# Kernel optimization log

Hardware: AMD Instinct MI355X
Metric: run time of the kernel (lower is better)

## Reference

```python
import jax, jax.numpy as jnp
import numpy as np

N = 4096            # number of proposals
C = 6               # classes incl. background
SCORE_TH = 0.05
NMS_TH = 0.3
DET_LIM = 100
IM_MAX = 1023.0     # clip to [0, im_size-1]
BBOX_W = jnp.array([10.0, 10.0, 10.0, 5.0, 5.0, 5.0], dtype=jnp.float32)


def setup_inputs() -> dict:
    key = jax.random.key(0)
    k1, k2, k3, k4 = jax.random.split(key, 4)
    # realistic 3D proposals inside the 1024^3 volume: lo in [0,900), size in [1,101)
    lo = jax.random.uniform(k1, (N, 3), dtype=jnp.float32) * 900.0
    sz = jax.random.uniform(k2, (N, 3), dtype=jnp.float32) * 100.0 + 1.0
    bbox_proposals = jnp.concatenate([jnp.zeros((N, 1), jnp.float32), lo, lo + sz], axis=1)  # [N,7]
    bbox_pred = jax.random.normal(k3, (N, C * 6), dtype=jnp.float32) * 0.1                   # [N,36]
    cls_score = jax.random.normal(k4, (N, C), dtype=jnp.float32)                              # [N,6]
    return {"bbox_proposals": bbox_proposals, "bbox_pred": bbox_pred, "cls_score": cls_score}


def _bbox_transform_clip(boxes, deltas):
    # boxes: [N,6] (x1,y1,z1,x2,y2,z2); deltas: [N, C*6] -> pred_boxes [N,C,6]
    d = deltas.reshape(N, C, 6) / BBOX_W
    sizes = boxes[:, 3:6] - boxes[:, 0:3] + 1.0          # [N,3]
    ctrs = boxes[:, 0:3] + 0.5 * sizes                   # [N,3]
    pred_ctr = d[:, :, :3] * sizes[:, None, :] + ctrs[:, None, :]
    pred_sz = jnp.exp(d[:, :, 3:]) * sizes[:, None, :]
    lo = jnp.clip(pred_ctr - 0.5 * pred_sz, 0.0, IM_MAX)
    hi = jnp.clip(pred_ctr + 0.5 * pred_sz - 1.0, 0.0, IM_MAX)
    return jnp.concatenate([lo, hi], axis=-1)            # [N,C,6]


def _nms_one_class(bj, sj):
    # bj: [N,6], sj: [N] -> scores with suppressed/below-threshold entries zeroed
    valid = sj > SCORE_TH
    order = jnp.argsort(-sj)
    b = bj[order]
    v = valid[order]
    l, h = b[:, :3], b[:, 3:]
    vol = jnp.prod(h - l + 1.0, axis=1)                                  # [N]
    inter = jnp.prod(
        jnp.clip(jnp.minimum(h[:, None, :], h[None, :, :])
                 - jnp.maximum(l[:, None, :], l[None, :, :]) + 1.0, 0.0, None),
        axis=-1)                                                          # [N,N]
    iou = inter / (vol[:, None] + vol[None, :] - inter)
    idx = jnp.arange(N)

    def body(i, keep):
        supp = keep[i] & (iou[i] > NMS_TH) & (idx > i)
        return keep & ~supp

    keep = jax.lax.fori_loop(0, N, body, v)
    keep_orig = jnp.zeros(N, bool).at[order].set(keep)
    return jnp.where(keep_orig, sj, 0.0)


def reference(bbox_proposals, bbox_pred, cls_score):
    scores = jax.nn.softmax(cls_score, axis=1)            # [N,C]
    boxes = bbox_proposals[:, 1:]                          # [N,6]
    pred_boxes = _bbox_transform_clip(boxes, bbox_pred)    # [N,C,6]
    cls_boxes = jnp.transpose(pred_boxes[:, 1:, :], (1, 0, 2))  # [5,N,6] (skip background)
    cls_scores = scores[:, 1:].T                                 # [5,N]
    kept = jax.vmap(_nms_one_class)(cls_boxes, cls_scores)       # [5,N]
    # top-100 detections-per-image limit (fixed-shape: zero out below image_thresh)
    thresh = jax.lax.top_k(kept.reshape(-1), DET_LIM)[0][-1]
    final = jnp.where(kept >= thresh, kept, 0.0)
    # pack boxes + final score: [5, N, 7]
    return jnp.concatenate([cls_boxes, final[:, :, None]], axis=-1)
```

## Files before the change

### kernel.cpp

```cpp
#include <hip/hip_runtime.h>
#include <stdint.h>

#define NN 4096
#define NCLS 5
#define NWORD 64
#define SCORE_TH 0.05f
#define NMS_TH 0.3f

__device__ __forceinline__ uint32_t fmap(float f) {
    uint32_t u = __float_as_uint(f);
    return (u & 0x80000000u) ? ~u : (u | 0x80000000u);
}
__device__ __forceinline__ float funmap(uint32_t m) {
    uint32_t u = (m & 0x80000000u) ? (m & 0x7fffffffu) : ~m;
    return __uint_as_float(u);
}

__global__ void k_prep(const float* __restrict__ prop, const float* __restrict__ pred,
                       const float* __restrict__ cls, float* __restrict__ out,
                       uint64_t* __restrict__ skey) {
    int i = blockIdx.x * 256 + threadIdx.x;
    if (i >= NN) return;
    const float* pr = prop + i * 7;
    float l0 = pr[1], l1 = pr[2], l2 = pr[3];
    float h0 = pr[4], h1 = pr[5], h2 = pr[6];
    float s0 = h0 - l0 + 1.f, s1 = h1 - l1 + 1.f, s2 = h2 - l2 + 1.f;
    float c0 = l0 + 0.5f * s0, c1 = l1 + 0.5f * s1, c2 = l2 + 0.5f * s2;

    float sc[6];
    float mx = -3.4e38f;
#pragma unroll
    for (int c = 0; c < 6; ++c) { sc[c] = cls[i * 6 + c]; mx = fmaxf(mx, sc[c]); }
    float sum = 0.f;
#pragma unroll
    for (int c = 0; c < 6; ++c) { sc[c] = expf(sc[c] - mx); sum += sc[c]; }
    float inv = 1.f / sum;

#pragma unroll
    for (int c = 1; c < 6; ++c) {
        const float* d = pred + i * 36 + c * 6;
        float dc0 = d[0] / 10.f, dc1 = d[1] / 10.f, dc2 = d[2] / 10.f;
        float ds0 = d[3] / 5.f, ds1 = d[4] / 5.f, ds2 = d[5] / 5.f;
        float pc0 = dc0 * s0 + c0, pc1 = dc1 * s1 + c1, pc2 = dc2 * s2 + c2;
        float ps0 = expf(ds0) * s0, ps1 = expf(ds1) * s1, ps2 = expf(ds2) * s2;
        float o0 = fminf(fmaxf(pc0 - 0.5f * ps0, 0.f), 1023.f);
        float o1 = fminf(fmaxf(pc1 - 0.5f * ps1, 0.f), 1023.f);
        float o2 = fminf(fmaxf(pc2 - 0.5f * ps2, 0.f), 1023.f);
        float o3 = fminf(fmaxf(pc0 + 0.5f * ps0 - 1.f, 0.f), 1023.f);
        float o4 = fminf(fmaxf(pc1 + 0.5f * ps1 - 1.f, 0.f), 1023.f);
        float o5 = fminf(fmaxf(pc2 + 0.5f * ps2 - 1.f, 0.f), 1023.f);
        float* ob = out + ((size_t)(c - 1) * NN + i) * 7;
        ob[0] = o0; ob[1] = o1; ob[2] = o2; ob[3] = o3; ob[4] = o4; ob[5] = o5;
        float score = sc[c] * inv;
        skey[(c - 1) * NN + i] = ((uint64_t)fmap(score) << 12) | (uint32_t)(4095 - i);
    }
}

__global__ void __launch_bounds__(256) k_sort(const uint64_t* __restrict__ skey,
                                              const float* __restrict__ out,
                                              float* __restrict__ sscores,
                                              unsigned short* __restrict__ order,
                                              float* __restrict__ sboxes) {
    int c = blockIdx.y;
    int i = blockIdx.x * 256 + threadIdx.x;
    const uint64_t* K = skey + c * NN;
    uint64_t ki = K[i];
    int rank = 0;
#pragma unroll 2
    for (int j = 0; j < NN; j += 8) {
        uint64_t k0 = K[j], k1 = K[j + 1], k2 = K[j + 2], k3 = K[j + 3];
        uint64_t k4 = K[j + 4], k5 = K[j + 5], k6 = K[j + 6], k7 = K[j + 7];
        int a = (k0 > ki) + (k1 > ki) + (k2 > ki) + (k3 > ki);
        int b = (k4 > ki) + (k5 > ki) + (k6 > ki) + (k7 > ki);
        rank += a + b;
    }
    int io = c * NN + rank;
    order[io] = (unsigned short)i;
    sscores[io] = funmap((uint32_t)(ki >> 12));
    const float* b = out + ((size_t)c * NN + i) * 7;
    float* sb = sboxes + (size_t)io * 6;
#pragma unroll
    for (int k = 0; k < 6; ++k) sb[k] = b[k];
}

__global__ void __launch_bounds__(256) k_mask(const float* __restrict__ sboxes,
                                              uint64_t* __restrict__ mask,
                                              uint64_t* __restrict__ diag) {
    int tid = threadIdx.x;
    int wid = tid >> 6, lane = tid & 63;
    int rb = blockIdx.y, c = blockIdx.z;
    int cb = rb + blockIdx.x * 4 + wid;
    bool active = (cb < 64);

    __shared__ float cB[4][64][6];
    __shared__ float cV[4][64];

    int r = rb * 64 + lane;
    float rl0 = 0, rl1 = 0, rl2 = 0, rh0 = 0, rh1 = 0, rh2 = 0, vi = 0;
    if (active) {
        const float* rp = sboxes + ((size_t)c * NN + r) * 6;
        rl0 = rp[0]; rl1 = rp[1]; rl2 = rp[2];
        rh0 = rp[3]; rh1 = rp[4]; rh2 = rp[5];
        vi = (rh0 - rl0 + 1.f) * (rh1 - rl1 + 1.f) * (rh2 - rl2 + 1.f);
        const float* cp = sboxes + ((size_t)c * NN + cb * 64 + lane) * 6;
#pragma unroll
        for (int k = 0; k < 6; ++k) cB[wid][lane][k] = cp[k];
        cV[wid][lane] = (cB[wid][lane][3] - cB[wid][lane][0] + 1.f) *
                        (cB[wid][lane][4] - cB[wid][lane][1] + 1.f) *
                        (cB[wid][lane][5] - cB[wid][lane][2] + 1.f);
    }
    __syncthreads();
    if (!active) return;

    uint64_t bits = 0;
    for (int j2 = 0; j2 < 64; ++j2) {
        int j = cb * 64 + j2;
        if (j > r) {
            float w0 = fmaxf(fminf(rh0, cB[wid][j2][3]) - fmaxf(rl0, cB[wid][j2][0]) + 1.f, 0.f);
            float w1 = fmaxf(fminf(rh1, cB[wid][j2][4]) - fmaxf(rl1, cB[wid][j2][1]) + 1.f, 0.f);
            float w2 = fmaxf(fminf(rh2, cB[wid][j2][5]) - fmaxf(rl2, cB[wid][j2][2]) + 1.f, 0.f);
            float inter = w0 * w1 * w2;
            float iou = inter / (vi + cV[wid][j2] - inter);
            if (iou > NMS_TH) bits |= 1ull << j2;
        }
    }
    mask[((size_t)c * NN + r) * NWORD + cb] = bits;
    if (cb == rb) diag[(size_t)c * NN + r] = bits;
}

__global__ void __launch_bounds__(64, 1) k_nms(const float* __restrict__ sscores,
                                               const unsigned short* __restrict__ order,
                                               const uint64_t* __restrict__ mask,
                                               const uint64_t* __restrict__ diag,
                                               float* __restrict__ kept) {
    __shared__ __align__(16) uint64_t ldiag[NN];
    __shared__ uint64_t sh[64];

    int c = blockIdx.x;
    int lane = threadIdx.x;
    const uint64_t* M = mask + (size_t)c * NN * NWORD;
    const uint64_t* D = diag + (size_t)c * NN;
    const float* ss = sscores + c * NN;

    {
        const uint4* g = (const uint4*)D;
        uint4* l = (uint4*)ldiag;
#pragma unroll 1
        for (int i = 0; i < 32; i += 8) {
            uint4 t0 = g[(i + 0) * 64 + lane], t1 = g[(i + 1) * 64 + lane];
            uint4 t2 = g[(i + 2) * 64 + lane], t3 = g[(i + 3) * 64 + lane];
            uint4 t4 = g[(i + 4) * 64 + lane], t5 = g[(i + 5) * 64 + lane];
            uint4 t6 = g[(i + 6) * 64 + lane], t7 = g[(i + 7) * 64 + lane];
            l[(i + 0) * 64 + lane] = t0; l[(i + 1) * 64 + lane] = t1;
            l[(i + 2) * 64 + lane] = t2; l[(i + 3) * 64 + lane] = t3;
            l[(i + 4) * 64 + lane] = t4; l[(i + 5) * 64 + lane] = t5;
            l[(i + 6) * 64 + lane] = t6; l[(i + 7) * 64 + lane] = t7;
        }
    }

    uint64_t remv = 0;
    {
        const float4* sl = (const float4*)(ss + lane * 64);
#pragma unroll
        for (int q = 0; q < 16; ++q) {
            float4 v = sl[q];
            if (!(v.x > SCORE_TH)) remv |= 1ull << (q * 4);
            if (!(v.y > SCORE_TH)) remv |= 1ull << (q * 4 + 1);
            if (!(v.z > SCORE_TH)) remv |= 1ull << (q * 4 + 2);
            if (!(v.w > SCORE_TH)) remv |= 1ull << (q * 4 + 3);
        }
    }
    __builtin_amdgcn_s_barrier();

#define ISSUE16(buf, base)                                          \
    _Pragma("unroll") for (int i_ = 0; i_ < 16; ++i_) {             \
        buf[i_] = R[(((base) + i_) << 6) | lane];                   \
    }

#define CHAIN16(base)                                               \
    {                                                               \
        uint32_t lo_[16], hi_[16];                                  \
        _Pragma("unroll") for (int b_ = 0; b_ < 16; ++b_) {         \
            lo_[b_] = __builtin_amdgcn_readlane(dgl, (base) + b_);  \
            hi_[b_] = __builtin_amdgcn_readlane(dgh, (base) + b_);  \
        }                                                           \
        _Pragma("unroll") for (int b_ = 0; b_ < 16; ++b_) {         \
            int bb_ = (base) + b_;                                  \
            if (!((rw >> bb_) & 1)) {                               \
                rw |= ((uint64_t)hi_[b_] << 32) | lo_[b_];          \
                kmask |= 1ull << bb_;                               \
            }                                                       \
        }                                                           \
    }

#define CONSUME16(buf, base, acc)                                   \
    _Pragma("unroll") for (int i_ = 0; i_ < 16; ++i_) {             \
        uint64_t kb_ = 0ull - ((kmask >> ((base) + i_)) & 1ull);    \
        acc |= buf[i_] & kb_;                                       \
    }

#pragma unroll 1
    for (int w = 0; w < 64; ++w) {
        const uint64_t* R = M + ((size_t)w << 12);
        uint64_t gA[16], gB[16];

        ISSUE16(gA, 0)
        ISSUE16(gB, 16)
        __builtin_amdgcn_sched_barrier(0);

        uint32_t rlo = __builtin_amdgcn_readlane((uint32_t)remv, w);
        uint32_t rhi = __builtin_amdgcn_readlane((uint32_t)(remv >> 32), w);
        uint64_t rw = ((uint64_t)rhi << 32) | rlo;
        uint64_t mydg = ldiag[(w << 6) | lane];
        uint32_t dgl = (uint32_t)mydg, dgh = (uint32_t)(mydg >> 32);
        uint64_t kmask = 0;
        uint64_t a0 = 0, a1 = 0, a2 = 0, a3 = 0;

        CHAIN16(0)
        CONSUME16(gA, 0, a0)
        ISSUE16(gA, 32)
        CHAIN16(16)
        CONSUME16(gB, 16, a1)
        ISSUE16(gB, 48)
        CHAIN16(32)
        CONSUME16(gA, 32, a2)
        CHAIN16(48)
        CONSUME16(gB, 48, a3)

        if (lane >= w) remv |= (a0 | a1) | (a2 | a3);
    }

#undef ISSUE16
#undef CHAIN16
#undef CONSUME16

    sh[lane] = remv;
    __syncthreads();
    const unsigned short* ord = order + c * NN;
    for (int t = 0; t < 64; ++t) {
        int p = t * 64 + lane;
        bool kp = !((sh[t] >> lane) & 1);
        float s = ss[p];
        int oi = ord[p];
        kept[c * NN + oi] = kp ? s : 0.f;
    }
}

__global__ void __launch_bounds__(1024) k_topk_final(const float* __restrict__ kept,
                                                     float* __restrict__ out) {
    int tid = threadIdx.x;
    uint32_t v[20];
#pragma unroll
    for (int k = 0; k < 20; ++k) v[k] = fmap(kept[k * 1024 + tid]);
    __shared__ int red[16];
    __shared__ int tot;
    uint32_t pre = 0;
    for (int bit = 31; bit >= 0; --bit) {
        uint32_t cand = pre | (1u << bit);
        int cnt = 0;
#pragma unroll
        for (int k = 0; k < 20; ++k) cnt += (v[k] >= cand);
#pragma unroll
        for (int off = 32; off; off >>= 1) cnt += __shfl_down(cnt, off, 64);
        if ((tid & 63) == 0) red[tid >> 6] = cnt;
        __syncthreads();
        if (tid == 0) {
            int s = 0;
            for (int q = 0; q < 16; ++q) s += red[q];
            tot = s;
        }
        __syncthreads();
        if (tot >= 100) pre = cand;
    }
#pragma unroll
    for (int k = 0; k < 20; ++k) {
        int idx = k * 1024 + tid;
        int c = idx >> 12;
        int i = idx & (NN - 1);
        out[((size_t)c * NN + i) * 7 + 6] = (v[k] >= pre) ? funmap(v[k]) : 0.f;
    }
}

extern "C" void kernel_launch(void* const* d_in, const int* in_sizes, int n_in,
                              void* d_out, int out_size, void* d_ws, size_t ws_size,
                              hipStream_t stream) {
    const float* prop = (const float*)d_in[0];
    const float* pred = (const float*)d_in[1];
    const float* cls = (const float*)d_in[2];
    float* out = (float*)d_out;

    char* base = (char*)d_ws;
    uint64_t* skey = (uint64_t*)base;
    uint64_t* diag = (uint64_t*)(base + (160ull << 10));
    float* sscores = (float*)(base + (320ull << 10));
    float* kept = (float*)(base + (400ull << 10));
    unsigned short* order = (unsigned short*)(base + (480ull << 10));
    float* sboxes = (float*)(base + (528ull << 10));
    uint64_t* mask = (uint64_t*)(base + (1ull << 20));

    k_prep<<<dim3(16), dim3(256), 0, stream>>>(prop, pred, cls, out, skey);
    k_sort<<<dim3(16, NCLS), dim3(256), 0, stream>>>(skey, out, sscores, order, sboxes);
    k_mask<<<dim3(16, 64, NCLS), dim3(256), 0, stream>>>(sboxes, mask, diag);
    k_nms<<<dim3(NCLS), dim3(64), 0, stream>>>(sscores, order, mask, diag, kept);
    k_topk_final<<<dim3(1), dim3(1024), 0, stream>>>(kept, out);
}
```

Before: 411.6 us.

## Split NMS bitmask scan across four wavefronts with LDS-shared keep mask

The serial NMS scan kernel now runs four wavefronts per class instead of one. Wave 0 resolves the 64-bit keep chain for each block, and all waves OR their own 16-row slice of the suppression mask. Partial suppression words pass through LDS slots, and each step prefetches the next block's mask rows. The goal is to spread mask loads and OR work over more waves and hide load latency. In exchange it adds two workgroup barriers per iteration on the serial critical path.

```diff
diff --git a/kernel.cpp b/kernel.cpp
--- a/kernel.cpp
+++ b/kernel.cpp
@@ -128,16 +128,27 @@
     if (cb == rb) diag[(size_t)c * NN + r] = bits;
 }
 
-__global__ void __launch_bounds__(64, 1) k_nms(const float* __restrict__ sscores,
-                                               const unsigned short* __restrict__ order,
-                                               const uint64_t* __restrict__ mask,
-                                               const uint64_t* __restrict__ diag,
-                                               float* __restrict__ kept) {
+#define NMS_BARRIER()                                        \
+    do {                                                     \
+        asm volatile("s_waitcnt lgkmcnt(0)" ::: "memory");   \
+        __builtin_amdgcn_s_barrier();                        \
+        asm volatile("" ::: "memory");                       \
+    } while (0)
+
+__global__ void __launch_bounds__(256, 1) k_nms(const float* __restrict__ sscores,
+                                                const unsigned short* __restrict__ order,
+                                                const uint64_t* __restrict__ mask,
+                                                const uint64_t* __restrict__ diag,
+                                                float* __restrict__ kept) {
     __shared__ __align__(16) uint64_t ldiag[NN];
+    __shared__ uint64_t slot[4];
+    __shared__ uint64_t pacc[4][64];
     __shared__ uint64_t sh[64];
-
+    __shared__ uint32_t km_sh[2];
+
+    int tid = threadIdx.x;
+    int wid = tid >> 6, lane = tid & 63;
     int c = blockIdx.x;
-    int lane = threadIdx.x;
     const uint64_t* M = mask + (size_t)c * NN * NWORD;
     const uint64_t* D = diag + (size_t)c * NN;
     const float* ss = sscores + c * NN;
@@ -145,37 +156,35 @@
     {
         const uint4* g = (const uint4*)D;
         uint4* l = (uint4*)ldiag;
-#pragma unroll 1
-        for (int i = 0; i < 32; i += 8) {
-            uint4 t0 = g[(i + 0) * 64 + lane], t1 = g[(i + 1) * 64 + lane];
-            uint4 t2 = g[(i + 2) * 64 + lane], t3 = g[(i + 3) * 64 + lane];
-            uint4 t4 = g[(i + 4) * 64 + lane], t5 = g[(i + 5) * 64 + lane];
-            uint4 t6 = g[(i + 6) * 64 + lane], t7 = g[(i + 7) * 64 + lane];
-            l[(i + 0) * 64 + lane] = t0; l[(i + 1) * 64 + lane] = t1;
-            l[(i + 2) * 64 + lane] = t2; l[(i + 3) * 64 + lane] = t3;
-            l[(i + 4) * 64 + lane] = t4; l[(i + 5) * 64 + lane] = t5;
-            l[(i + 6) * 64 + lane] = t6; l[(i + 7) * 64 + lane] = t7;
-        }
-    }
-
-    uint64_t remv = 0;
-    {
+        uint4 t0 = g[(wid * 8 + 0) * 64 + lane], t1 = g[(wid * 8 + 1) * 64 + lane];
+        uint4 t2 = g[(wid * 8 + 2) * 64 + lane], t3 = g[(wid * 8 + 3) * 64 + lane];
+        uint4 t4 = g[(wid * 8 + 4) * 64 + lane], t5 = g[(wid * 8 + 5) * 64 + lane];
+        uint4 t6 = g[(wid * 8 + 6) * 64 + lane], t7 = g[(wid * 8 + 7) * 64 + lane];
+        l[(wid * 8 + 0) * 64 + lane] = t0; l[(wid * 8 + 1) * 64 + lane] = t1;
+        l[(wid * 8 + 2) * 64 + lane] = t2; l[(wid * 8 + 3) * 64 + lane] = t3;
+        l[(wid * 8 + 4) * 64 + lane] = t4; l[(wid * 8 + 5) * 64 + lane] = t5;
+        l[(wid * 8 + 6) * 64 + lane] = t6; l[(wid * 8 + 7) * 64 + lane] = t7;
+    }
+
+    uint64_t initW = 0;
+    if (wid == 0) {
         const float4* sl = (const float4*)(ss + lane * 64);
 #pragma unroll
         for (int q = 0; q < 16; ++q) {
             float4 v = sl[q];
-            if (!(v.x > SCORE_TH)) remv |= 1ull << (q * 4);
-            if (!(v.y > SCORE_TH)) remv |= 1ull << (q * 4 + 1);
-            if (!(v.z > SCORE_TH)) remv |= 1ull << (q * 4 + 2);
-            if (!(v.w > SCORE_TH)) remv |= 1ull << (q * 4 + 3);
-        }
-    }
-    __builtin_amdgcn_s_barrier();
-
-#define ISSUE16(buf, base)                                          \
-    _Pragma("unroll") for (int i_ = 0; i_ < 16; ++i_) {             \
-        buf[i_] = R[(((base) + i_) << 6) | lane];                   \
-    }
+            if (!(v.x > SCORE_TH)) initW |= 1ull << (q * 4);
+            if (!(v.y > SCORE_TH)) initW |= 1ull << (q * 4 + 1);
+            if (!(v.z > SCORE_TH)) initW |= 1ull << (q * 4 + 2);
+            if (!(v.w > SCORE_TH)) initW |= 1ull << (q * 4 + 3);
+        }
+    }
+    if (tid < 4) slot[tid] = 0;
+
+    uint64_t g0[16];
+#pragma unroll
+    for (int i = 0; i < 16; ++i) g0[i] = M[((wid * 16 + i) << 6) | lane];
+
+    NMS_BARRIER();
 
 #define CHAIN16(base)                                               \
     {                                                               \
@@ -193,51 +202,55 @@
         }                                                           \
     }
 
-#define CONSUME16(buf, base, acc)                                   \
-    _Pragma("unroll") for (int i_ = 0; i_ < 16; ++i_) {             \
-        uint64_t kb_ = 0ull - ((kmask >> ((base) + i_)) & 1ull);    \
-        acc |= buf[i_] & kb_;                                       \
-    }
-
+    uint64_t racc = 0;
 #pragma unroll 1
     for (int w = 0; w < 64; ++w) {
-        const uint64_t* R = M + ((size_t)w << 12);
-        uint64_t gA[16], gB[16];
-
-        ISSUE16(gA, 0)
-        ISSUE16(gB, 16)
-        __builtin_amdgcn_sched_barrier(0);
-
-        uint32_t rlo = __builtin_amdgcn_readlane((uint32_t)remv, w);
-        uint32_t rhi = __builtin_amdgcn_readlane((uint32_t)(remv >> 32), w);
-        uint64_t rw = ((uint64_t)rhi << 32) | rlo;
-        uint64_t mydg = ldiag[(w << 6) | lane];
-        uint32_t dgl = (uint32_t)mydg, dgh = (uint32_t)(mydg >> 32);
-        uint64_t kmask = 0;
-        uint64_t a0 = 0, a1 = 0, a2 = 0, a3 = 0;
-
-        CHAIN16(0)
-        CONSUME16(gA, 0, a0)
-        ISSUE16(gA, 32)
-        CHAIN16(16)
-        CONSUME16(gB, 16, a1)
-        ISSUE16(gB, 48)
-        CHAIN16(32)
-        CONSUME16(gA, 32, a2)
-        CHAIN16(48)
-        CONSUME16(gB, 48, a3)
-
-        if (lane >= w) remv |= (a0 | a1) | (a2 | a3);
-    }
-
-#undef ISSUE16
+        if (wid == 0) {
+            uint32_t ilo = __builtin_amdgcn_readlane((uint32_t)initW, w);
+            uint32_t ihi = __builtin_amdgcn_readlane((uint32_t)(initW >> 32), w);
+            uint64_t rw = (((uint64_t)ihi << 32) | ilo) |
+                          slot[0] | slot[1] | slot[2] | slot[3];
+            uint64_t mydg = ldiag[(w << 6) | lane];
+            uint32_t dgl = (uint32_t)mydg, dgh = (uint32_t)(mydg >> 32);
+            uint64_t kmask = 0;
+            CHAIN16(0) CHAIN16(16) CHAIN16(32) CHAIN16(48)
+            if (lane == 0) {
+                km_sh[0] = (uint32_t)kmask;
+                km_sh[1] = (uint32_t)(kmask >> 32);
+            }
+        }
+        NMS_BARRIER();
+
+        uint64_t kmask = ((uint64_t)km_sh[1] << 32) | km_sh[0];
+        uint64_t a = 0;
+#pragma unroll
+        for (int i = 0; i < 16; ++i) {
+            uint64_t kb = 0ull - ((kmask >> (wid * 16 + i)) & 1ull);
+            a |= g0[i] & kb;
+        }
+        if (lane >= w) racc |= a;
+
+        if (w < 63) {
+            const uint64_t* R = M + ((size_t)(w + 1) << 12);
+#pragma unroll
+            for (int i = 0; i < 16; ++i) g0[i] = R[((wid * 16 + i) << 6) | lane];
+            uint32_t plo = __builtin_amdgcn_readlane((uint32_t)racc, w + 1);
+            uint32_t phi = __builtin_amdgcn_readlane((uint32_t)(racc >> 32), w + 1);
+            if (lane == 0) slot[wid] = ((uint64_t)phi << 32) | plo;
+        }
+        NMS_BARRIER();
+    }
 #undef CHAIN16
-#undef CONSUME16
-
-    sh[lane] = remv;
-    __syncthreads();
+
+    pacc[wid][lane] = racc;
+    NMS_BARRIER();
+    if (wid == 0)
+        sh[lane] = initW | pacc[0][lane] | pacc[1][lane] | pacc[2][lane] | pacc[3][lane];
+    NMS_BARRIER();
     const unsigned short* ord = order + c * NN;
-    for (int t = 0; t < 64; ++t) {
+#pragma unroll
+    for (int tt = 0; tt < 16; ++tt) {
+        int t = wid * 16 + tt;
         int p = t * 64 + lane;
         bool kp = !((sh[t] >> lane) & 1);
         float s = ss[p];
@@ -301,6 +314,6 @@
     k_prep<<<dim3(16), dim3(256), 0, stream>>>(prop, pred, cls, out, skey);
     k_sort<<<dim3(16, NCLS), dim3(256), 0, stream>>>(skey, out, sscores, order, sboxes);
     k_mask<<<dim3(16, 64, NCLS), dim3(256), 0, stream>>>(sboxes, mask, diag);
-    k_nms<<<dim3(NCLS), dim3(64), 0, stream>>>(sscores, order, mask, diag, kept);
+    k_nms<<<dim3(NCLS), dim3(256), 0, stream>>>(sscores, order, mask, diag, kept);
     k_topk_final<<<dim3(1), dim3(1024), 0, stream>>>(kept, out);
 }
```

Measured after the change: 393.3 us. 1.05x faster.
